# Performance work log

Hardware: AMD Instinct MI355X
Metric: run time of the kernel (lower is better)

Reference implementation:

```python
import jax, jax.numpy as jnp
import numpy as np
from jax import lax

NUM_HEADS = 8
EPS_BN = 1e-5
EPS_LN = 1e-5


def setup_inputs() -> dict:
    key = jax.random.key(0)
    ks = iter(jax.random.split(key, 32))
    C = 512
    R = C // 16  # channel-gate reduction
    HID = 512    # classifier hidden
    NC = 1       # num_classes

    def gn(shape, scale=0.02):
        return (jax.random.normal(next(ks), shape, dtype=jnp.float32) * scale)

    inp = {
        "x": jax.random.normal(next(ks), (16, C, 28, 28), dtype=jnp.float32),
        # ChannelGate MLP (Linear(C,R) -> ReLU -> Linear(R,C))
        "mlp_w1": gn((R, C)), "mlp_b1": jnp.zeros((R,), jnp.float32),
        "mlp_w2": gn((C, R)), "mlp_b2": jnp.zeros((C,), jnp.float32),
        # SpatialGate 7x7 conv (2->1, no bias) + BatchNorm2d(1) eval-mode stats
        "sp_w": gn((1, 2, 7, 7)),
        "sp_gamma": jnp.ones((1,), jnp.float32), "sp_beta": jnp.zeros((1,), jnp.float32),
        "sp_mean": jnp.zeros((1,), jnp.float32), "sp_var": jnp.ones((1,), jnp.float32),
        # attention projections
        "wq": gn((C, C)), "bq": jnp.zeros((C,), jnp.float32),
        "wk": gn((C, C)), "bk": jnp.zeros((C,), jnp.float32),
        "wv": gn((C, C)), "bv": jnp.zeros((C,), jnp.float32),
        "wo": gn((C, C)), "bo": jnp.zeros((C,), jnp.float32),
        # classifier: LayerNorm(C) -> Linear(C,512) -> ReLU -> Linear(512,NC)
        "ln_g": jnp.ones((C,), jnp.float32), "ln_b": jnp.zeros((C,), jnp.float32),
        "fc1_w": gn((HID, C)), "fc1_b": jnp.zeros((HID,), jnp.float32),
        "fc2_w": gn((NC, HID)), "fc2_b": jnp.zeros((NC,), jnp.float32),
    }
    return inp


def reference(x, mlp_w1, mlp_b1, mlp_w2, mlp_b2, sp_w, sp_gamma, sp_beta,
              sp_mean, sp_var, wq, bq, wk, bk, wv, bv, wo, bo,
              ln_g, ln_b, fc1_w, fc1_b, fc2_w, fc2_b):
    B, C, H, W = x.shape
    N = H * W
    hd = C // NUM_HEADS

    # ---- CBAM: channel gate (avg + max global pools through shared MLP) ----
    def mlp(p):  # p: [B, C]
        return jax.nn.relu(p @ mlp_w1.T + mlp_b1) @ mlp_w2.T + mlp_b2

    avg_p = x.mean(axis=(2, 3))
    max_p = x.max(axis=(2, 3))
    ch_scale = jax.nn.sigmoid(mlp(avg_p) + mlp(max_p))[:, :, None, None]
    x = x * ch_scale

    # ---- CBAM: spatial gate ----
    comp = jnp.concatenate([x.max(axis=1, keepdims=True),
                            x.mean(axis=1, keepdims=True)], axis=1)  # [B,2,H,W]
    s = lax.conv_general_dilated(comp, sp_w, window_strides=(1, 1),
                                 padding=[(3, 3), (3, 3)],
                                 dimension_numbers=("NCHW", "OIHW", "NCHW"))
    s = (s - sp_mean[None, :, None, None]) * lax.rsqrt(sp_var + EPS_BN)[None, :, None, None]
    s = s * sp_gamma[None, :, None, None] + sp_beta[None, :, None, None]
    x = x * jax.nn.sigmoid(s)

    # ---- multi-head self-attention over HW tokens ----
    xf = x.reshape(B, C, N).transpose(0, 2, 1)  # [B, N, C]

    def heads(w, b):
        return (xf @ w.T + b).reshape(B, N, NUM_HEADS, hd).transpose(0, 2, 1, 3)

    Q, K, V = heads(wq, bq), heads(wk, bk), heads(wv, bv)  # [B, h, N, d]
    scores = jnp.einsum("bhnd,bhmd->bhnm", Q, K) / jnp.sqrt(jnp.float32(hd))
    attn = jax.nn.softmax(scores, axis=-1)  # dropout is identity in eval
    attended = jnp.einsum("bhnm,bhmd->bhnd", attn, V)
    attended = attended.transpose(0, 2, 1, 3).reshape(B, N, C)
    attended = attended @ wo.T + bo
    x = x + attended.transpose(0, 2, 1).reshape(B, C, H, W)

    # ---- classifier head ----
    p = x.mean(axis=(2, 3))  # AdaptiveAvgPool2d(1) + Flatten -> [B, C]
    mu = p.mean(axis=-1, keepdims=True)
    var = p.var(axis=-1, keepdims=True)
    ln = (p - mu) * lax.rsqrt(var + EPS_LN) * ln_g + ln_b
    h = jax.nn.relu(ln @ fc1_w.T + fc1_b)
    return h @ fc2_w.T + fc2_b
```

## Files before the change

kernel.cpp:

```cpp
#include <hip/hip_runtime.h>
#include <math.h>

#define BB 16
#define CC 512
#define HW 784
#define RR 32
#define NHD 8
#define HD 64
#define NT 784
#define NTILE 49
#define SROW 20

#define OFS_AVGP   0
#define OFS_MAXP   8192
#define OFS_CHS    16384
#define OFS_CMAX   24576
#define OFS_CMEAN  37120
#define OFS_SP     49664
#define OFS_P1     62208
#define OFS_ABAR   70400
#define OFS_XG     78592
#define XG_SZ      (BB*CC*HW)
#define OFS_XGT    (OFS_XG + XG_SZ)
#define OFS_QBF    (OFS_XGT + XG_SZ/2)
#define OFS_KBF    (OFS_QBF + XG_SZ/2)
#define OFS_V2     (OFS_KBF + XG_SZ/2)
#define OFS_WF     (OFS_V2 + XG_SZ)
#define OFS_W      OFS_XG
#define OFS_PV     (OFS_XG + 131072)
#define OFS_LNV    (OFS_PV + 8192)
#define OFS_H1     (OFS_LNV + 8192)
#define OFS_CMAXP  (OFS_XG + 262144)
#define OFS_CMEANP (OFS_CMAXP + 200704)

typedef __attribute__((ext_vector_type(8))) short bf16x8;
typedef __attribute__((ext_vector_type(4))) float f32x4;

__device__ __forceinline__ unsigned short f2bf(float x) {
  union { float f; unsigned u; } v; v.f = x;
  unsigned r = v.u + 0x7fffu + ((v.u >> 16) & 1u);
  return (unsigned short)(r >> 16);
}
__device__ __forceinline__ float bf2f(unsigned short x) {
  union { unsigned u; float f; } v; v.u = ((unsigned)x) << 16;
  return v.f;
}

__global__ void k_pool(const float* __restrict__ x, float* avg_p, float* max_p) {
  int wid = threadIdx.x >> 6;
  int lane = threadIdx.x & 63;
  int row = blockIdx.x * 4 + wid;
  const float* xr = x + (size_t)row * HW;
  float s = 0.f, m = -INFINITY;
  for (int i = lane; i < HW; i += 64) { float v = xr[i]; s += v; m = fmaxf(m, v); }
  for (int o = 32; o; o >>= 1) { s += __shfl_down(s, o, 64); m = fmaxf(m, __shfl_down(m, o, 64)); }
  if (lane == 0) { avg_p[row] = s * (1.f/HW); max_p[row] = m; }
}

__global__ void k_chmlp(const float* avg_p, const float* max_p,
                        const float* w1, const float* b1,
                        const float* w2, const float* b2, float* chs) {
  __shared__ float pa[CC], pm[CC], part[256], hr[64];
  int b = blockIdx.x, t = threadIdx.x;
  for (int i = t; i < CC; i += 256) { pa[i] = avg_p[b*CC+i]; pm[i] = max_p[b*CC+i]; }
  __syncthreads();
  {
    int rp = t & 63, ch = t >> 6;
    int r = rp & 31;
    const float* src = (rp < 32) ? pa : pm;
    const float* wr = w1 + (size_t)r*CC + ch*128;
    float s = 0.f;
    #pragma unroll 8
    for (int c = 0; c < 128; c++) s += src[ch*128 + c] * wr[c];
    part[t] = s;
  }
  __syncthreads();
  if (t < 64)
    hr[t] = fmaxf(part[t] + part[64+t] + part[128+t] + part[192+t] + b1[t & 31], 0.f);
  __syncthreads();
  for (int c = t; c < CC; c += 256) {
    float a = 2.f*b2[c];
    const float* wr = w2 + c*RR;
    #pragma unroll
    for (int r = 0; r < RR; r++) a += (hr[r]+hr[32+r])*wr[r];
    chs[b*CC+c] = 1.f/(1.f+__expf(-a));
  }
}

__global__ void k_chgatep(const float* __restrict__ x, const float* __restrict__ chs,
                          float* __restrict__ cmaxp, float* __restrict__ cmeanp) {
  __shared__ float cs[32];
  int b = blockIdx.x, cg = blockIdx.y, t = threadIdx.x;
  if (t < 32) cs[t] = chs[b*CC + cg*32 + t];
  __syncthreads();
  const float* xb = x + ((size_t)b*CC + cg*32)*HW;
  for (int pix = t; pix < HW; pix += 256) {
    float mx = -INFINITY, sm = 0.f;
    #pragma unroll
    for (int c = 0; c < 32; c++) {
      float v = xb[(size_t)c*HW + pix] * cs[c];
      mx = fmaxf(mx, v); sm += v;
    }
    cmaxp[(size_t)(cg*BB + b)*HW + pix] = mx;
    cmeanp[(size_t)(cg*BB + b)*HW + pix] = sm;
  }
}

__global__ void k_cred(const float* __restrict__ cmaxp, const float* __restrict__ cmeanp,
                       float* __restrict__ cmax, float* __restrict__ cmean) {
  int idx = blockIdx.x*256 + threadIdx.x;
  if (idx >= BB*HW) return;
  int b = idx / HW, pix = idx % HW;
  float mx = -INFINITY, sm = 0.f;
  #pragma unroll
  for (int cg = 0; cg < 16; cg++) {
    mx = fmaxf(mx, cmaxp[(size_t)(cg*BB + b)*HW + pix]);
    sm += cmeanp[(size_t)(cg*BB + b)*HW + pix];
  }
  cmax[idx] = mx; cmean[idx] = sm * (1.f/CC);
}

__global__ void k_spconv(const float* __restrict__ cmax, const float* __restrict__ cmean,
                         const float* __restrict__ w,
                         const float* g, const float* be, const float* mu, const float* var,
                         float* sp) {
  int b = blockIdx.x;
  int pix = blockIdx.y*256 + threadIdx.x;
  if (pix >= HW) return;
  int h = pix/28, wd = pix%28;
  float acc = 0.f;
  for (int kh = 0; kh < 7; kh++) {
    int ih = h + kh - 3; if (ih < 0 || ih >= 28) continue;
    for (int kw = 0; kw < 7; kw++) {
      int iw = wd + kw - 3; if (iw < 0 || iw >= 28) continue;
      int ip = ih*28+iw;
      acc += cmax[b*HW+ip]*w[kh*7+kw] + cmean[b*HW+ip]*w[49+kh*7+kw];
    }
  }
  float s = (acc - mu[0])*rsqrtf(var[0]+1e-5f)*g[0] + be[0];
  sp[b*HW+pix] = 1.f/(1.f+__expf(-s));
}

__global__ void k_sfuse(const float* __restrict__ x, const float* __restrict__ chs,
                        const float* __restrict__ sp, unsigned short* __restrict__ xgT,
                        float* __restrict__ p1) {
  __shared__ float cs[CC];
  int nt = blockIdx.x, b = blockIdx.y;
  int t = threadIdx.x, ln = t & 63;
  for (int i = t; i < CC; i += 256) cs[i] = chs[b*CC+i];
  __syncthreads();
  int n = nt*16 + (ln & 15);
  float spv = sp[b*HW + n];
  const float* xb = x + (size_t)b*CC*HW;
  #pragma unroll
  for (int i = 0; i < 4; i++) {
    int s = (t >> 6) + 4*i;
    int c = s*32 + (ln >> 4)*8;
    float v[8]; bf16x8 p;
    #pragma unroll
    for (int j = 0; j < 8; j++) {
      v[j] = xb[(size_t)(c+j)*HW + n] * cs[c+j] * spv;
      p[j] = (short)f2bf(v[j]);
    }
    *(bf16x8*)(xgT + ((((size_t)b*NTILE + nt)*16 + s)*64 + ln)*8) = p;
    #pragma unroll
    for (int j = 0; j < 8; j++) {
      float sv = v[j];
      sv += __shfl_xor(sv, 1, 64); sv += __shfl_xor(sv, 2, 64);
      sv += __shfl_xor(sv, 4, 64); sv += __shfl_xor(sv, 8, 64);
      if ((ln & 15) == 0) atomicAdd(&p1[b*CC + c + j], sv * (1.f/HW));
    }
  }
}

__global__ void k_wfrag(const float* __restrict__ wq, const float* __restrict__ wk,
                        const float* __restrict__ wv, unsigned short* __restrict__ Wf) {
  int idx = blockIdx.x*256 + threadIdx.x;
  int ln = idx & 63;
  int s  = (idx >> 6) & 15;
  int ct = (idx >> 10) & 31;
  int mat = idx >> 15;
  const float* W = (mat==0)? wq : (mat==1)? wk : wv;
  const float* src = W + (size_t)(ct*16 + (ln & 15))*CC + s*32 + (ln >> 4)*8;
  float4 f0 = *(const float4*)src;
  float4 f1 = *(const float4*)(src + 4);
  bf16x8 p;
  p[0]=(short)f2bf(f0.x); p[1]=(short)f2bf(f0.y); p[2]=(short)f2bf(f0.z); p[3]=(short)f2bf(f0.w);
  p[4]=(short)f2bf(f1.x); p[5]=(short)f2bf(f1.y); p[6]=(short)f2bf(f1.z); p[7]=(short)f2bf(f1.w);
  *(bf16x8*)(Wf + (size_t)idx*8) = p;
}

__global__ __launch_bounds__(256) void k_qkv_mfma(
    const unsigned short* __restrict__ xgT, const unsigned short* __restrict__ Wf,
    const float* __restrict__ bq, const float* __restrict__ bk, const float* __restrict__ bv,
    unsigned short* __restrict__ Qbf, unsigned short* __restrict__ Kbf,
    unsigned short* __restrict__ Vbf) {
  __shared__ float Cb[64*132];
  int mt = blockIdx.x;
  int yb = blockIdx.y;
  int b  = blockIdx.z;
  int mat = yb >> 2;
  int c0 = (yb & 3) * 128;
  int t = threadIdx.x, w = t >> 6, ln = t & 63;
  const unsigned short* Ab = xgT + (size_t)b*NTILE*8192;
  const unsigned short* Bb = Wf + (size_t)mat*32*8192;
  int ctg0 = (c0 >> 4) + w*2;
  f32x4 acc[4][2];
  #pragma unroll
  for (int m = 0; m < 4; m++)
    #pragma unroll
    for (int c2 = 0; c2 < 2; c2++) acc[m][c2] = (f32x4){0.f,0.f,0.f,0.f};
  int ntc[4];
  #pragma unroll
  for (int m = 0; m < 4; m++) { int nt = 4*mt + m; ntc[m] = (nt > 48) ? 48 : nt; }
  for (int s = 0; s < 16; s++) {
    bf16x8 bf0 = *(const bf16x8*)(Bb + (size_t)(ctg0*16 + s)*512 + ln*8);
    bf16x8 bf1 = *(const bf16x8*)(Bb + (size_t)((ctg0+1)*16 + s)*512 + ln*8);
    bf16x8 af[4];
    #pragma unroll
    for (int m = 0; m < 4; m++)
      af[m] = *(const bf16x8*)(Ab + (size_t)(ntc[m]*16 + s)*512 + ln*8);
    #pragma unroll
    for (int m = 0; m < 4; m++) {
      acc[m][0] = __builtin_amdgcn_mfma_f32_16x16x32_bf16(af[m], bf0, acc[m][0], 0,0,0);
      acc[m][1] = __builtin_amdgcn_mfma_f32_16x16x32_bf16(af[m], bf1, acc[m][1], 0,0,0);
    }
  }
  #pragma unroll
  for (int m = 0; m < 4; m++)
    #pragma unroll
    for (int c2 = 0; c2 < 2; c2++)
      #pragma unroll
      for (int r = 0; r < 4; r++)
        Cb[(m*16 + (ln>>4)*4 + r)*132 + w*32 + c2*16 + (ln&15)] = acc[m][c2][r];
  __syncthreads();
  const float* bias = (mat==0)? bq : (mat==1)? bk : bv;
  #pragma unroll
  for (int i = 0; i < 4; i++) {
    int p = w*4 + i;
    int ntl = p >> 2, sl = p & 3;
    int nt = 4*mt + ntl;
    if (nt > 48) continue;
    int row = ntl*16 + (ln & 15);
    int col = sl*32 + (ln >> 4)*8;
    float v[8];
    #pragma unroll
    for (int j = 0; j < 8; j++) v[j] = Cb[row*132 + col + j] + bias[c0 + col + j];
    int token = nt*16 + (ln & 15);
    int h = (c0 >> 6) + (sl >> 1);
    int bh = b*NHD + h;
    bf16x8 pk;
    #pragma unroll
    for (int j = 0; j < 8; j++) pk[j] = (short)f2bf(v[j]);
    if (mat < 2) {
      unsigned short* Out = (mat == 0) ? Qbf : Kbf;
      *(bf16x8*)(Out + ((size_t)bh*NTILE + nt)*1024 + (size_t)(sl & 1)*512 + ln*8) = pk;
    } else {
      int d = (sl & 1)*32 + (ln >> 4)*8;
      *(bf16x8*)(Vbf + ((size_t)bh*NT + token)*HD + d) = pk;
    }
  }
}

__global__ __launch_bounds__(256, 2) void k_attn5(const unsigned short* __restrict__ Qbf,
    const unsigned short* __restrict__ Kbf, float* __restrict__ wsum) {
  __shared__ float Se[NTILE*16*SROW];
  __shared__ float l_tmp[64];
  __shared__ float rl[16];
  int bh = blockIdx.x & 127, nt = blockIdx.x >> 7;
  int t = threadIdx.x, w = t >> 6, ln = t & 63;
  const unsigned short* Qb = Qbf + ((size_t)bh*NTILE + nt)*1024;
  const unsigned short* Kb = Kbf + (size_t)bh*NTILE*1024;
  bf16x8 q0 = *(const bf16x8*)(Qb + ln*8);
  bf16x8 q1 = *(const bf16x8*)(Qb + 512 + ln*8);
  float lp[4] = {0.f,0.f,0.f,0.f};
  for (int mt = w; mt < NTILE; mt += 4) {
    bf16x8 k0 = *(const bf16x8*)(Kb + (size_t)mt*1024 + ln*8);
    bf16x8 k1 = *(const bf16x8*)(Kb + (size_t)mt*1024 + 512 + ln*8);
    f32x4 a = {0.f,0.f,0.f,0.f};
    a = __builtin_amdgcn_mfma_f32_16x16x32_bf16(q0, k0, a, 0,0,0);
    a = __builtin_amdgcn_mfma_f32_16x16x32_bf16(q1, k1, a, 0,0,0);
    int m = mt*16 + (ln & 15);
    f32x4 ev;
    #pragma unroll
    for (int r = 0; r < 4; r++) {
      ev[r] = __expf(a[r]*0.125f);
      lp[r] += ev[r];
    }
    *(f32x4*)&Se[m*SROW + (ln>>4)*4] = ev;
  }
  #pragma unroll
  for (int r = 0; r < 4; r++) {
    float v = lp[r];
    v += __shfl_xor(v,1,64); v += __shfl_xor(v,2,64);
    v += __shfl_xor(v,4,64); v += __shfl_xor(v,8,64);
    if ((ln & 15) == 0) l_tmp[w*16 + (ln>>4)*4 + r] = v;
  }
  __syncthreads();
  if (t < 16) rl[t] = 1.f / (l_tmp[t] + l_tmp[16+t] + l_tmp[32+t] + l_tmp[48+t]);
  __syncthreads();
  f32x4 rlv[4];
  #pragma unroll
  for (int j = 0; j < 4; j++) rlv[j] = *(const f32x4*)&rl[j*4];
  for (int m = t; m < NT; m += 256) {
    const float* row = &Se[m*SROW];
    float s = 0.f;
    #pragma unroll
    for (int j = 0; j < 4; j++) {
      f32x4 e = *(const f32x4*)&row[j*4];
      s += e[0]*rlv[j][0] + e[1]*rlv[j][1] + e[2]*rlv[j][2] + e[3]*rlv[j][3];
    }
    atomicAdd(&wsum[bh*NT + m], s);
  }
}

__global__ void k_attn_av(const float* __restrict__ w, const unsigned short* __restrict__ Vm,
                          float* __restrict__ abar) {
  __shared__ float red[256];
  int bh = blockIdx.x, t = threadIdx.x;
  int d = t & 63, chunk = t >> 6;
  float acc = 0.f;
  const unsigned short* vb = Vm + (size_t)bh*NT*HD;
  const float* wb = w + bh*NT;
  for (int m = chunk*196; m < (chunk+1)*196; m++)
    acc += wb[m] * bf2f(vb[(size_t)m*HD + d]);
  red[t] = acc;
  __syncthreads();
  if (t < 64)
    abar[bh*HD + t] = (red[t] + red[64+t] + red[128+t] + red[192+t]) * (1.f/NT);
}

__global__ void k_headA(const float* __restrict__ p1, const float* __restrict__ abar,
                        const float* __restrict__ wo, const float* __restrict__ bo,
                        float* __restrict__ pv) {
  int b = blockIdx.x, cg = blockIdx.y;
  int t = threadIdx.x, w = t >> 6, ln = t & 63;
  float a[8];
  #pragma unroll
  for (int k = 0; k < 8; k++) a[k] = abar[b*CC + ln + 64*k];
  int c0 = cg*64 + w*16;
  for (int i = 0; i < 16; i++) {
    int c = c0 + i;
    const float* wr = wo + (size_t)c*CC;
    float s = 0.f;
    #pragma unroll
    for (int k = 0; k < 8; k++) s += a[k] * wr[ln + 64*k];
    for (int o = 32; o; o >>= 1) s += __shfl_down(s, o, 64);
    if (ln == 0) pv[b*CC + c] = s + bo[c] + p1[b*CC + c];
  }
}

__global__ void k_headB(const float* __restrict__ pv, const float* __restrict__ ln_g,
                        const float* __restrict__ ln_b, float* __restrict__ lnv) {
  int b = blockIdx.x, ln = threadIdx.x;
  float v[8], s = 0.f, s2 = 0.f;
  #pragma unroll
  for (int k = 0; k < 8; k++) { v[k] = pv[b*CC + ln + 64*k]; s += v[k]; s2 += v[k]*v[k]; }
  for (int o = 32; o; o >>= 1) { s += __shfl_down(s, o, 64); s2 += __shfl_down(s2, o, 64); }
  s = __shfl(s, 0, 64); s2 = __shfl(s2, 0, 64);
  float mean = s * (1.f/CC);
  float rs = rsqrtf(s2*(1.f/CC) - mean*mean + 1e-5f);
  #pragma unroll
  for (int k = 0; k < 8; k++) {
    int c = ln + 64*k;
    lnv[b*CC + c] = (v[k]-mean)*rs*ln_g[c] + ln_b[c];
  }
}

__global__ void k_headC(const float* __restrict__ lnv, const float* __restrict__ fc1_w,
                        const float* __restrict__ fc1_b, float* __restrict__ h1) {
  int b = blockIdx.x, cg = blockIdx.y;
  int t = threadIdx.x, w = t >> 6, ln = t & 63;
  float a[8];
  #pragma unroll
  for (int k = 0; k < 8; k++) a[k] = lnv[b*CC + ln + 64*k];
  int c0 = cg*64 + w*16;
  for (int i = 0; i < 16; i++) {
    int c = c0 + i;
    const float* wr = fc1_w + (size_t)c*CC;
    float s = 0.f;
    #pragma unroll
    for (int k = 0; k < 8; k++) s += a[k] * wr[ln + 64*k];
    for (int o = 32; o; o >>= 1) s += __shfl_down(s, o, 64);
    if (ln == 0) h1[b*CC + c] = fmaxf(s + fc1_b[c], 0.f);
  }
}

__global__ void k_headD(const float* __restrict__ h1, const float* __restrict__ fc2_w,
                        const float* __restrict__ fc2_b, float* __restrict__ out) {
  int b = blockIdx.x, ln = threadIdx.x;
  float s = 0.f;
  #pragma unroll
  for (int k = 0; k < 8; k++) s += h1[b*CC + ln + 64*k] * fc2_w[ln + 64*k];
  for (int o = 32; o; o >>= 1) s += __shfl_down(s, o, 64);
  if (ln == 0) out[b] = s + fc2_b[0];
}

extern "C" void kernel_launch(void* const* d_in, const int* in_sizes, int n_in,
                              void* d_out, int out_size, void* d_ws, size_t ws_size,
                              hipStream_t stream) {
  const float* x       = (const float*)d_in[0];
  const float* mlp_w1  = (const float*)d_in[1];
  const float* mlp_b1  = (const float*)d_in[2];
  const float* mlp_w2  = (const float*)d_in[3];
  const float* mlp_b2  = (const float*)d_in[4];
  const float* sp_w    = (const float*)d_in[5];
  const float* sp_g    = (const float*)d_in[6];
  const float* sp_b    = (const float*)d_in[7];
  const float* sp_mu   = (const float*)d_in[8];
  const float* sp_var  = (const float*)d_in[9];
  const float* wq      = (const float*)d_in[10];
  const float* bq      = (const float*)d_in[11];
  const float* wk      = (const float*)d_in[12];
  const float* bk      = (const float*)d_in[13];
  const float* wv      = (const float*)d_in[14];
  const float* bv      = (const float*)d_in[15];
  const float* wo      = (const float*)d_in[16];
  const float* bo      = (const float*)d_in[17];
  const float* ln_g    = (const float*)d_in[18];
  const float* ln_b    = (const float*)d_in[19];
  const float* fc1_w   = (const float*)d_in[20];
  const float* fc1_b   = (const float*)d_in[21];
  const float* fc2_w   = (const float*)d_in[22];
  const float* fc2_b   = (const float*)d_in[23];

  float* ws = (float*)d_ws;
  float* avg_p = ws + OFS_AVGP;
  float* max_p = ws + OFS_MAXP;
  float* chs   = ws + OFS_CHS;
  float* cmax  = ws + OFS_CMAX;
  float* cmean = ws + OFS_CMEAN;
  float* sp    = ws + OFS_SP;
  float* p1    = ws + OFS_P1;
  float* abar  = ws + OFS_ABAR;
  unsigned short* xgT = (unsigned short*)(ws + OFS_XGT);
  unsigned short* Qbf = (unsigned short*)(ws + OFS_QBF);
  unsigned short* Kbf = (unsigned short*)(ws + OFS_KBF);
  unsigned short* Vbf = (unsigned short*)(ws + OFS_V2);
  unsigned short* Wf  = (unsigned short*)(ws + OFS_WF);
  float* wsum  = ws + OFS_W;
  float* pv    = ws + OFS_PV;
  float* lnv   = ws + OFS_LNV;
  float* h1    = ws + OFS_H1;
  float* cmaxp = ws + OFS_CMAXP;
  float* cmeanp= ws + OFS_CMEANP;

  hipMemsetAsync(p1, 0, BB*CC*sizeof(float), stream);
  hipMemsetAsync(wsum, 0, BB*NHD*NT*sizeof(float), stream);

  k_pool   <<<2048, 256, 0, stream>>>(x, avg_p, max_p);
  k_chmlp  <<<BB, 256, 0, stream>>>(avg_p, max_p, mlp_w1, mlp_b1, mlp_w2, mlp_b2, chs);
  k_chgatep<<<dim3(BB,16), 256, 0, stream>>>(x, chs, cmaxp, cmeanp);
  k_cred   <<<49, 256, 0, stream>>>(cmaxp, cmeanp, cmax, cmean);
  k_spconv <<<dim3(BB,4), 256, 0, stream>>>(cmax, cmean, sp_w, sp_g, sp_b, sp_mu, sp_var, sp);
  k_wfrag  <<<384, 256, 0, stream>>>(wq, wk, wv, Wf);
  k_sfuse  <<<dim3(NTILE,BB), 256, 0, stream>>>(x, chs, sp, xgT, p1);
  k_qkv_mfma<<<dim3(13,12,BB), 256, 0, stream>>>(xgT, Wf, bq, bk, bv, Qbf, Kbf, Vbf);
  k_attn5  <<<NTILE*128, 256, 0, stream>>>(Qbf, Kbf, wsum);
  k_attn_av<<<128, 256, 0, stream>>>(wsum, Vbf, abar);
  k_headA  <<<dim3(BB,8), 256, 0, stream>>>(p1, abar, wo, bo, pv);
  k_headB  <<<BB, 64, 0, stream>>>(pv, ln_g, ln_b, lnv);
  k_headC  <<<dim3(BB,8), 256, 0, stream>>>(lnv, fc1_w, fc1_b, h1);
  k_headD  <<<BB, 64, 0, stream>>>(h1, fc2_w, fc2_b, (float*)d_out);
}
```

Baseline: 318.9 us.

## Keep attention exps in registers, fuse channel reduce with spatial conv, remap QKV grid

The attention-weight kernel now keeps the exponentiated scores in registers instead of a large shared-memory buffer. It reduces across lanes with shuffles and issues one atomic per column from 16 lanes, and it raises the occupancy hint from 2 to 5 blocks per CU. The channel-pool reduction and the 7x7 spatial conv are merged into one kernel that stages the maps in shared memory, removing a launch and a global round trip. The QKV GEMM moves to a flat grid ordered batch-fastest, uses an odd shared-memory stride to avoid bank conflicts, and unrolls its K loop by two. The trade-off is higher register pressure in the attention kernel and only 16 blocks for the fused conv.

```diff
diff --git a/kernel.cpp b/kernel.cpp
--- a/kernel.cpp
+++ b/kernel.cpp
@@ -9,7 +9,7 @@
 #define HD 64
 #define NT 784
 #define NTILE 49
-#define SROW 20
+#define CBS 131
 
 #define OFS_AVGP   0
 #define OFS_MAXP   8192
@@ -106,39 +106,36 @@
   }
 }
 
-__global__ void k_cred(const float* __restrict__ cmaxp, const float* __restrict__ cmeanp,
-                       float* __restrict__ cmax, float* __restrict__ cmean) {
-  int idx = blockIdx.x*256 + threadIdx.x;
-  if (idx >= BB*HW) return;
-  int b = idx / HW, pix = idx % HW;
-  float mx = -INFINITY, sm = 0.f;
-  #pragma unroll
-  for (int cg = 0; cg < 16; cg++) {
-    mx = fmaxf(mx, cmaxp[(size_t)(cg*BB + b)*HW + pix]);
-    sm += cmeanp[(size_t)(cg*BB + b)*HW + pix];
-  }
-  cmax[idx] = mx; cmean[idx] = sm * (1.f/CC);
-}
-
-__global__ void k_spconv(const float* __restrict__ cmax, const float* __restrict__ cmean,
-                         const float* __restrict__ w,
-                         const float* g, const float* be, const float* mu, const float* var,
-                         float* sp) {
-  int b = blockIdx.x;
-  int pix = blockIdx.y*256 + threadIdx.x;
-  if (pix >= HW) return;
-  int h = pix/28, wd = pix%28;
-  float acc = 0.f;
-  for (int kh = 0; kh < 7; kh++) {
-    int ih = h + kh - 3; if (ih < 0 || ih >= 28) continue;
-    for (int kw = 0; kw < 7; kw++) {
-      int iw = wd + kw - 3; if (iw < 0 || iw >= 28) continue;
-      int ip = ih*28+iw;
-      acc += cmax[b*HW+ip]*w[kh*7+kw] + cmean[b*HW+ip]*w[49+kh*7+kw];
-    }
-  }
-  float s = (acc - mu[0])*rsqrtf(var[0]+1e-5f)*g[0] + be[0];
-  sp[b*HW+pix] = 1.f/(1.f+__expf(-s));
+__global__ void k_credsp(const float* __restrict__ cmaxp, const float* __restrict__ cmeanp,
+                         const float* __restrict__ w, const float* g, const float* be,
+                         const float* mu, const float* var, float* __restrict__ sp) {
+  __shared__ float cmx[HW], cmn[HW];
+  int b = blockIdx.x, t = threadIdx.x;
+  for (int pix = t; pix < HW; pix += 256) {
+    float mx = -INFINITY, sm = 0.f;
+    #pragma unroll
+    for (int cg = 0; cg < 16; cg++) {
+      mx = fmaxf(mx, cmaxp[(size_t)(cg*BB + b)*HW + pix]);
+      sm += cmeanp[(size_t)(cg*BB + b)*HW + pix];
+    }
+    cmx[pix] = mx; cmn[pix] = sm * (1.f/CC);
+  }
+  __syncthreads();
+  float bnscale = rsqrtf(var[0]+1e-5f)*g[0];
+  for (int pix = t; pix < HW; pix += 256) {
+    int h = pix/28, wd = pix%28;
+    float acc = 0.f;
+    for (int kh = 0; kh < 7; kh++) {
+      int ih = h + kh - 3; if (ih < 0 || ih >= 28) continue;
+      for (int kw = 0; kw < 7; kw++) {
+        int iw = wd + kw - 3; if (iw < 0 || iw >= 28) continue;
+        int ip = ih*28+iw;
+        acc += cmx[ip]*w[kh*7+kw] + cmn[ip]*w[49+kh*7+kw];
+      }
+    }
+    float s = (acc - mu[0])*bnscale + be[0];
+    sp[b*HW+pix] = 1.f/(1.f+__expf(-s));
+  }
 }
 
 __global__ void k_sfuse(const float* __restrict__ x, const float* __restrict__ chs,
@@ -195,10 +192,12 @@
     const float* __restrict__ bq, const float* __restrict__ bk, const float* __restrict__ bv,
     unsigned short* __restrict__ Qbf, unsigned short* __restrict__ Kbf,
     unsigned short* __restrict__ Vbf) {
-  __shared__ float Cb[64*132];
-  int mt = blockIdx.x;
-  int yb = blockIdx.y;
-  int b  = blockIdx.z;
+  __shared__ float Cb[64*CBS];
+  int blk = blockIdx.x;
+  int yb = blk / 208;
+  int r0 = blk % 208;
+  int mt = r0 >> 4;
+  int b  = r0 & 15;
   int mat = yb >> 2;
   int c0 = (yb & 3) * 128;
   int t = threadIdx.x, w = t >> 6, ln = t & 63;
@@ -213,6 +212,7 @@
   int ntc[4];
   #pragma unroll
   for (int m = 0; m < 4; m++) { int nt = 4*mt + m; ntc[m] = (nt > 48) ? 48 : nt; }
+  #pragma unroll 2
   for (int s = 0; s < 16; s++) {
     bf16x8 bf0 = *(const bf16x8*)(Bb + (size_t)(ctg0*16 + s)*512 + ln*8);
     bf16x8 bf1 = *(const bf16x8*)(Bb + (size_t)((ctg0+1)*16 + s)*512 + ln*8);
@@ -232,7 +232,7 @@
     for (int c2 = 0; c2 < 2; c2++)
       #pragma unroll
       for (int r = 0; r < 4; r++)
-        Cb[(m*16 + (ln>>4)*4 + r)*132 + w*32 + c2*16 + (ln&15)] = acc[m][c2][r];
+        Cb[(m*16 + (ln>>4)*4 + r)*CBS + w*32 + c2*16 + (ln&15)] = acc[m][c2][r];
   __syncthreads();
   const float* bias = (mat==0)? bq : (mat==1)? bk : bv;
   #pragma unroll
@@ -245,7 +245,7 @@
     int col = sl*32 + (ln >> 4)*8;
     float v[8];
     #pragma unroll
-    for (int j = 0; j < 8; j++) v[j] = Cb[row*132 + col + j] + bias[c0 + col + j];
+    for (int j = 0; j < 8; j++) v[j] = Cb[row*CBS + col + j] + bias[c0 + col + j];
     int token = nt*16 + (ln & 15);
     int h = (c0 >> 6) + (sl >> 1);
     int bh = b*NHD + h;
@@ -262,9 +262,8 @@
   }
 }
 
-__global__ __launch_bounds__(256, 2) void k_attn5(const unsigned short* __restrict__ Qbf,
+__global__ __launch_bounds__(256, 5) void k_attn7(const unsigned short* __restrict__ Qbf,
     const unsigned short* __restrict__ Kbf, float* __restrict__ wsum) {
-  __shared__ float Se[NTILE*16*SROW];
   __shared__ float l_tmp[64];
   __shared__ float rl[16];
   int bh = blockIdx.x & 127, nt = blockIdx.x >> 7;
@@ -273,21 +272,26 @@
   const unsigned short* Kb = Kbf + (size_t)bh*NTILE*1024;
   bf16x8 q0 = *(const bf16x8*)(Qb + ln*8);
   bf16x8 q1 = *(const bf16x8*)(Qb + 512 + ln*8);
+  f32x4 ev[13];
   float lp[4] = {0.f,0.f,0.f,0.f};
-  for (int mt = w; mt < NTILE; mt += 4) {
-    bf16x8 k0 = *(const bf16x8*)(Kb + (size_t)mt*1024 + ln*8);
-    bf16x8 k1 = *(const bf16x8*)(Kb + (size_t)mt*1024 + 512 + ln*8);
+  #pragma unroll
+  for (int i = 0; i < 13; i++) {
+    int mt = w + 4*i;
+    bool valid = (i < 12) || (w == 0);
+    int mtc = valid ? mt : 48;
+    bf16x8 k0 = *(const bf16x8*)(Kb + (size_t)mtc*1024 + ln*8);
+    bf16x8 k1 = *(const bf16x8*)(Kb + (size_t)mtc*1024 + 512 + ln*8);
     f32x4 a = {0.f,0.f,0.f,0.f};
     a = __builtin_amdgcn_mfma_f32_16x16x32_bf16(q0, k0, a, 0,0,0);
     a = __builtin_amdgcn_mfma_f32_16x16x32_bf16(q1, k1, a, 0,0,0);
-    int m = mt*16 + (ln & 15);
-    f32x4 ev;
-    #pragma unroll
-    for (int r = 0; r < 4; r++) {
-      ev[r] = __expf(a[r]*0.125f);
-      lp[r] += ev[r];
-    }
-    *(f32x4*)&Se[m*SROW + (ln>>4)*4] = ev;
+    f32x4 e;
+    #pragma unroll
+    for (int r = 0; r < 4; r++) e[r] = __expf(a[r]*0.125f);
+    ev[i] = e;
+    if (valid) {
+      #pragma unroll
+      for (int r = 0; r < 4; r++) lp[r] += e[r];
+    }
   }
   #pragma unroll
   for (int r = 0; r < 4; r++) {
@@ -299,18 +303,16 @@
   __syncthreads();
   if (t < 16) rl[t] = 1.f / (l_tmp[t] + l_tmp[16+t] + l_tmp[32+t] + l_tmp[48+t]);
   __syncthreads();
-  f32x4 rlv[4];
-  #pragma unroll
-  for (int j = 0; j < 4; j++) rlv[j] = *(const f32x4*)&rl[j*4];
-  for (int m = t; m < NT; m += 256) {
-    const float* row = &Se[m*SROW];
-    float s = 0.f;
-    #pragma unroll
-    for (int j = 0; j < 4; j++) {
-      f32x4 e = *(const f32x4*)&row[j*4];
-      s += e[0]*rlv[j][0] + e[1]*rlv[j][1] + e[2]*rlv[j][2] + e[3]*rlv[j][3];
-    }
-    atomicAdd(&wsum[bh*NT + m], s);
+  f32x4 rlq = *(const f32x4*)&rl[(ln >> 4)*4];
+  #pragma unroll
+  for (int i = 0; i < 13; i++) {
+    int mt = w + 4*i;
+    bool valid = (i < 12) || (w == 0);
+    float v = ev[i][0]*rlq[0] + ev[i][1]*rlq[1] + ev[i][2]*rlq[2] + ev[i][3]*rlq[3];
+    v += __shfl_xor(v, 16, 64);
+    v += __shfl_xor(v, 32, 64);
+    if (valid && ln < 16)
+      atomicAdd(&wsum[bh*NT + mt*16 + ln], v);
   }
 }
 
@@ -428,8 +430,6 @@
   float* avg_p = ws + OFS_AVGP;
   float* max_p = ws + OFS_MAXP;
   float* chs   = ws + OFS_CHS;
-  float* cmax  = ws + OFS_CMAX;
-  float* cmean = ws + OFS_CMEAN;
   float* sp    = ws + OFS_SP;
   float* p1    = ws + OFS_P1;
   float* abar  = ws + OFS_ABAR;
@@ -451,12 +451,11 @@
   k_pool   <<<2048, 256, 0, stream>>>(x, avg_p, max_p);
   k_chmlp  <<<BB, 256, 0, stream>>>(avg_p, max_p, mlp_w1, mlp_b1, mlp_w2, mlp_b2, chs);
   k_chgatep<<<dim3(BB,16), 256, 0, stream>>>(x, chs, cmaxp, cmeanp);
-  k_cred   <<<49, 256, 0, stream>>>(cmaxp, cmeanp, cmax, cmean);
-  k_spconv <<<dim3(BB,4), 256, 0, stream>>>(cmax, cmean, sp_w, sp_g, sp_b, sp_mu, sp_var, sp);
+  k_credsp <<<BB, 256, 0, stream>>>(cmaxp, cmeanp, sp_w, sp_g, sp_b, sp_mu, sp_var, sp);
   k_wfrag  <<<384, 256, 0, stream>>>(wq, wk, wv, Wf);
   k_sfuse  <<<dim3(NTILE,BB), 256, 0, stream>>>(x, chs, sp, xgT, p1);
-  k_qkv_mfma<<<dim3(13,12,BB), 256, 0, stream>>>(xgT, Wf, bq, bk, bv, Qbf, Kbf, Vbf);
-  k_attn5  <<<NTILE*128, 256, 0, stream>>>(Qbf, Kbf, wsum);
+  k_qkv_mfma<<<2496, 256, 0, stream>>>(xgT, Wf, bq, bk, bv, Qbf, Kbf, Vbf);
+  k_attn7  <<<NTILE*128, 256, 0, stream>>>(Qbf, Kbf, wsum);
   k_attn_av<<<128, 256, 0, stream>>>(wsum, Vbf, abar);
   k_headA  <<<dim3(BB,8), 256, 0, stream>>>(p1, abar, wo, bo, pv);
   k_headB  <<<BB, 64, 0, stream>>>(pv, ln_g, ln_b, lnv);
```

Measured after the change: 291.8 us. 1.09x faster.
